# Performance work log

Measured on AMD Instinct MI355X. Metric: run time of the kernel, lower is better.

Reference implementation:

```python
import jax, jax.numpy as jnp
import numpy as np

B, L, D, H = 4, 2048, 1024, 16
HD = D // H


def setup_inputs() -> dict:
    key = jax.random.key(0)
    k0, k1, k2, k3, k4 = jax.random.split(key, 5)
    scale = 1.0 / np.sqrt(D)
    x = jax.random.normal(k0, (B, L, D), dtype=jnp.float32)
    Wk = jax.random.normal(k1, (D, D), dtype=jnp.float32) * scale
    Wv = jax.random.normal(k2, (D, D), dtype=jnp.float32) * scale
    Wr = jax.random.normal(k3, (D, D), dtype=jnp.float32) * scale
    Wo = jax.random.normal(k4, (D, D), dtype=jnp.float32) * scale
    # time_decay init: geometric decay per head, broadcast over head_dim
    decay = jnp.exp(-5.0 * jnp.arange(1, H + 1, dtype=jnp.float32) / H)
    time_decay = jnp.broadcast_to(decay[:, None], (H, HD)).astype(jnp.float32)
    time_first = jnp.full((H, HD), 0.5, dtype=jnp.float32)
    return {"x": x, "Wk": Wk, "Wv": Wv, "Wr": Wr, "Wo": Wo,
            "time_decay": time_decay, "time_first": time_first}


def reference(x, Wk, Wv, Wr, Wo, time_decay, time_first):
    b, l, d = x.shape
    h, hd = time_decay.shape
    # projections (nn.Linear: x @ W.T)
    k = (x @ Wk.T).reshape(b, l, h, hd)
    v = (x @ Wv.T).reshape(b, l, h, hd)
    r = jax.nn.sigmoid(x @ Wr.T).reshape(b, l, h, hd)

    decay = time_decay[None, :, :, None]   # (1,H,HD,1) broadcast over 'e' axis
    tf = time_first[None, :, :, None]      # (1,H,HD,1)

    def step(state, inp):
        k_t, v_t, r_t = inp                 # each (B,H,HD)
        # state: (B,H,HD,HD); outer product k_t (d) x v_t (e)
        state = state * decay + (k_t[..., :, None] * v_t[..., None, :]) * tf
        y_t = jnp.einsum('bhde,bhd->bhe', state, r_t)
        return state, y_t

    state0 = jnp.zeros((b, h, hd, hd), dtype=x.dtype)
    seq = (jnp.moveaxis(k, 1, 0), jnp.moveaxis(v, 1, 0), jnp.moveaxis(r, 1, 0))
    final_state, ys = jax.lax.scan(step, state0, seq)   # ys: (L,B,H,HD)
    y = jnp.moveaxis(ys, 0, 1).reshape(b, l, d) @ Wo.T
    return y, final_state
```

## Files before the change

kernel.cpp:

```cpp
#include <hip/hip_runtime.h>

typedef unsigned short u16;
typedef unsigned int   u32;
typedef __attribute__((ext_vector_type(8))) short bfrag;
typedef __attribute__((ext_vector_type(4))) float ffrag;

#define MFMA16(a,b,c) __builtin_amdgcn_mfma_f32_16x16x32_bf16((a),(b),(c),0,0,0)

#define GLL16(gp, lp) __builtin_amdgcn_global_load_lds( \
    (const __attribute__((address_space(1))) u32*)(gp), \
    (__attribute__((address_space(3))) u32*)(lp), 16, 0, 0)

__device__ __forceinline__ u16 f2b(float f) {
  u32 u = __float_as_uint(f);
  return (u16)((u + 0x7fffu + ((u >> 16) & 1u)) >> 16);
}
__device__ __forceinline__ float b2f(u16 v) { return __uint_as_float(((u32)v) << 16); }

__device__ __forceinline__ void unpack8(uint4 q, u16 e[8]) {
  e[0] = q.x & 0xffffu; e[1] = q.x >> 16;
  e[2] = q.y & 0xffffu; e[3] = q.y >> 16;
  e[4] = q.z & 0xffffu; e[5] = q.z >> 16;
  e[6] = q.w & 0xffffu; e[7] = q.w >> 16;
}

__global__ __launch_bounds__(256) void cvt_all(
    const float* __restrict__ x,  const float* __restrict__ wk,
    const float* __restrict__ wv, const float* __restrict__ wr,
    const float* __restrict__ wo,
    u16* __restrict__ xb, u16* __restrict__ wb, u16* __restrict__ wob)
{
  size_t i4 = ((size_t)blockIdx.x * 256 + threadIdx.x) * 4;
  const float* src; u16* dst; size_t off;
  if      (i4 <  8388608) { src = x;  dst = xb;            off = i4; }
  else if (i4 <  9437184) { src = wk; dst = wb;            off = i4 - 8388608; }
  else if (i4 < 10485760) { src = wv; dst = wb + 1048576;  off = i4 - 9437184; }
  else if (i4 < 11534336) { src = wr; dst = wb + 2097152;  off = i4 - 10485760; }
  else                    { src = wo; dst = wob;           off = i4 - 11534336; }
  float4 f = *(const float4*)(src + off);
  u16 o[4] = { f2b(f.x), f2b(f.y), f2b(f.z), f2b(f.w) };
  *(ushort4*)(dst + off) = make_ushort4(o[0], o[1], o[2], o[3]);
}

__global__ __launch_bounds__(512, 4) void k1_proj(
    const u16* __restrict__ xb, const u16* __restrict__ wb,
    const float* __restrict__ tf,
    u16* __restrict__ kws, u16* __restrict__ vws, u16* __restrict__ rws)
{
  __shared__ u16 As[2][256 * 32];
  __shared__ u16 Bs[2][128 * 32];
  const int tid  = threadIdx.x;
  const int wave = tid >> 6, lane = tid & 63;
  const int li = lane & 15, quad = lane >> 4;
  const int wm = (wave >> 1) * 64, wn = (wave & 1) * 64;

  const int bid = blockIdx.x;
  const int xcd = bid & 7, j = bid >> 3;
  const int n0 = (j >> 2) * 128;
  const int m0 = ((xcd << 2) | (j & 3)) * 256;

  ffrag acc[4][4];
#pragma unroll
  for (int i = 0; i < 4; ++i)
#pragma unroll
    for (int jj = 0; jj < 4; ++jj)
#pragma unroll
      for (int r = 0; r < 4; ++r) acc[i][jj][r] = 0.f;

  const int sr = lane >> 2, sc = (lane & 3) * 8;
  const u16* ga0 = xb + (size_t)(m0 + wave * 32 + sr) * 1024 + sc;
  const u16* gb0 = wb + (size_t)(n0 + wave * 16 + sr) * 1024 + sc;

  GLL16(ga0,             As[0] + wave * 1024);
  GLL16(ga0 + 16 * 1024, As[0] + wave * 1024 + 512);
  GLL16(gb0,             Bs[0] + wave * 512);

  for (int it = 0; it < 32; ++it) {
    __syncthreads();
    if (it + 1 < 32) {
      const int nb = (it + 1) & 1;
      const u16* ga = ga0 + (it + 1) * 32;
      const u16* gb = gb0 + (it + 1) * 32;
      GLL16(ga,             As[nb] + wave * 1024);
      GLL16(ga + 16 * 1024, As[nb] + wave * 1024 + 512);
      GLL16(gb,             Bs[nb] + wave * 512);
    }
    const int cb = it & 1;
    bfrag av[4], bv[4];
#pragma unroll
    for (int i = 0; i < 4; ++i)  av[i]  = *(const bfrag*)&As[cb][(wm + i * 16 + li) * 32 + quad * 8];
#pragma unroll
    for (int jj = 0; jj < 4; ++jj) bv[jj] = *(const bfrag*)&Bs[cb][(wn + jj * 16 + li) * 32 + quad * 8];
#pragma unroll
    for (int i = 0; i < 4; ++i)
#pragma unroll
      for (int jj = 0; jj < 4; ++jj)
        acc[i][jj] = MFMA16(av[i], bv[jj], acc[i][jj]);
  }

  const int sel = n0 >> 10;
#pragma unroll
  for (int i = 0; i < 4; ++i) {
#pragma unroll
    for (int jj = 0; jj < 4; ++jj) {
#pragma unroll
      for (int r = 0; r < 4; ++r) {
        int m = m0 + wm + i * 16 + quad * 4 + r;
        int n = n0 + wn + jj * 16 + li;
        int c = n & 1023;
        int bb = m >> 11, l = m & 2047;
        size_t dst = (size_t)((bb << 4) | (c >> 6)) * 131072 + (size_t)l * 64 + (c & 63);
        float v = acc[i][jj][r];
        if (sel == 0)      kws[dst] = f2b(v * tf[c]);
        else if (sel == 1) vws[dst] = f2b(v);
        else               rws[dst] = f2b(1.f / (1.f + __expf(-v)));
      }
    }
  }
}

#define ST 72

__global__ __launch_bounds__(256) void k2a_u(
    const u16* __restrict__ kws, const u16* __restrict__ vws,
    const float* __restrict__ td, u16* __restrict__ ut)
{
  __shared__ u16 KbarT[64 * ST];
  __shared__ u16 Vt[64 * ST];
  const int tid = threadIdx.x;
  const int lane = tid & 63, wave = tid >> 6;
  const int li = lane & 15, quad = lane >> 4;
  const int wr = (wave >> 1) * 32, wc = (wave & 1) * 32;
  const int bid = blockIdx.x;
  const int bh = bid >> 5, ch = bid & 31;
  const int h = bh & 15;
  const float l2D = log2f(td[h * 64]);
  const size_t base = (size_t)bh * 131072 + (size_t)ch * 4096;

#pragma unroll
  for (int it = 0; it < 2; ++it) {
    int c16 = tid + it * 256;
    int row = c16 >> 3, c8 = (c16 & 7) * 8;
    size_t g = base + (size_t)row * 64 + c8;
    uint4 kq = *(const uint4*)(kws + g);
    u16 ke[8]; unpack8(kq, ke);
    float sk = exp2f((float)(63 - row) * l2D);
#pragma unroll
    for (int jj = 0; jj < 8; ++jj) KbarT[(c8 + jj) * ST + row] = f2b(b2f(ke[jj]) * sk);
    uint4 vq = *(const uint4*)(vws + g);
    u16 ve[8]; unpack8(vq, ve);
#pragma unroll
    for (int jj = 0; jj < 8; ++jj) Vt[(c8 + jj) * ST + row] = ve[jj];
  }
  __syncthreads();

  ffrag U[2][2];
#pragma unroll
  for (int a = 0; a < 2; ++a)
#pragma unroll
    for (int b = 0; b < 2; ++b)
#pragma unroll
      for (int r = 0; r < 4; ++r) U[a][b][r] = 0.f;
#pragma unroll
  for (int kk = 0; kk < 64; kk += 32) {
    bfrag a0 = *(const bfrag*)&Vt[(wr + li) * ST + kk + quad * 8];
    bfrag a1 = *(const bfrag*)&Vt[(wr + 16 + li) * ST + kk + quad * 8];
    bfrag b0 = *(const bfrag*)&KbarT[(wc + li) * ST + kk + quad * 8];
    bfrag b1 = *(const bfrag*)&KbarT[(wc + 16 + li) * ST + kk + quad * 8];
    U[0][0] = MFMA16(a0, b0, U[0][0]);
    U[0][1] = MFMA16(a0, b1, U[0][1]);
    U[1][0] = MFMA16(a1, b0, U[1][0]);
    U[1][1] = MFMA16(a1, b1, U[1][1]);
  }

  u16* dst = ut + ((size_t)bid << 12);
#pragma unroll
  for (int ti = 0; ti < 2; ++ti)
#pragma unroll
    for (int tj = 0; tj < 2; ++tj)
#pragma unroll
      for (int r = 0; r < 4; ++r) {
        int e = wr + ti * 16 + quad * 4 + r;
        int d = wc + tj * 16 + li;
        dst[e * 64 + d] = f2b(U[ti][tj][r]);
      }
}

__global__ __launch_bounds__(256) void k2b_scan(
    const u16* __restrict__ ut, const float* __restrict__ td,
    u16* __restrict__ sbf, float* __restrict__ fstate)
{
  __shared__ float Sl[4 * 65];
  const int tid = threadIdx.x;
  const int bid = blockIdx.x;
  const int bh = bid >> 4, q = bid & 15;
  const int ed = q * 256 + tid;
  const int h = bh & 15;
  const float Dh = td[h * 64];
  const float DhC = exp2f(64.f * log2f(Dh));

  float S = 0.f;
  size_t idx = ((size_t)bh * 32) * 4096 + ed;
  for (int c = 0; c < 32; ++c, idx += 4096) {
    sbf[idx] = f2b(S);
    S = S * DhC + b2f(ut[idx]);
  }
  Sl[(tid >> 6) * 65 + (tid & 63)] = S;
  __syncthreads();
  int d = tid >> 2, el = tid & 3;
  fstate[(size_t)bh * 4096 + (size_t)d * 64 + q * 4 + el] = Sl[el * 65 + d];
}

__global__ __launch_bounds__(256) void k2c_y(
    const u16* __restrict__ kws, const u16* __restrict__ vws, const u16* __restrict__ rws,
    const u16* __restrict__ sbf, const float* __restrict__ td,
    u16* __restrict__ yws)
{
  __shared__ u16 Rc[64 * ST];
  __shared__ u16 KcA[64 * ST];
  __shared__ u16 Vt[64 * ST];
  __shared__ u16 STc[64 * ST];
  __shared__ float Dpow[65];

  const int tid = threadIdx.x;
  const int lane = tid & 63, wave = tid >> 6;
  const int li = lane & 15, quad = lane >> 4;
  const int wr = (wave >> 1) * 32, wc = (wave & 1) * 32;
  const int bid = blockIdx.x;
  const int bh = bid >> 5, ch = bid & 31;
  const int h = bh & 15, bb = bh >> 4;
  const float l2D = log2f(td[h * 64]);
  if (tid <= 64) Dpow[tid] = exp2f((float)tid * l2D);

  const size_t base = (size_t)bh * 131072 + (size_t)ch * 4096;
  const u16* sp = sbf + ((size_t)bid << 12);

#pragma unroll
  for (int it = 0; it < 2; ++it) {
    int c16 = tid + it * 256;
    int row = c16 >> 3, c8 = (c16 & 7) * 8;
    size_t g = base + (size_t)row * 64 + c8;
    *(uint4*)&Rc[row * ST + c8]  = *(const uint4*)(rws + g);
    *(uint4*)&KcA[row * ST + c8] = *(const uint4*)(kws + g);
    *(uint4*)&STc[row * ST + c8] = *(const uint4*)(sp + (size_t)row * 64 + c8);
    uint4 vq = *(const uint4*)(vws + g);
    u16 ve[8]; unpack8(vq, ve);
#pragma unroll
    for (int jj = 0; jj < 8; ++jj) Vt[(c8 + jj) * ST + row] = ve[jj];
  }
  __syncthreads();

  ffrag P[2][2], Y[2][2];
#pragma unroll
  for (int a = 0; a < 2; ++a)
#pragma unroll
    for (int b = 0; b < 2; ++b)
#pragma unroll
      for (int r = 0; r < 4; ++r) { P[a][b][r] = 0.f; Y[a][b][r] = 0.f; }

#pragma unroll
  for (int kk = 0; kk < 64; kk += 32) {
    bfrag a0 = *(const bfrag*)&Rc[(wr + li) * ST + kk + quad * 8];
    bfrag a1 = *(const bfrag*)&Rc[(wr + 16 + li) * ST + kk + quad * 8];
    bfrag b0 = *(const bfrag*)&KcA[(wc + li) * ST + kk + quad * 8];
    bfrag b1 = *(const bfrag*)&KcA[(wc + 16 + li) * ST + kk + quad * 8];
    P[0][0] = MFMA16(a0, b0, P[0][0]);
    P[0][1] = MFMA16(a0, b1, P[0][1]);
    P[1][0] = MFMA16(a1, b0, P[1][0]);
    P[1][1] = MFMA16(a1, b1, P[1][1]);
    bfrag s0 = *(const bfrag*)&STc[(wc + li) * ST + kk + quad * 8];
    bfrag s1 = *(const bfrag*)&STc[(wc + 16 + li) * ST + kk + quad * 8];
    Y[0][0] = MFMA16(a0, s0, Y[0][0]);
    Y[0][1] = MFMA16(a0, s1, Y[0][1]);
    Y[1][0] = MFMA16(a1, s0, Y[1][0]);
    Y[1][1] = MFMA16(a1, s1, Y[1][1]);
  }

#pragma unroll
  for (int ti = 0; ti < 2; ++ti)
#pragma unroll
    for (int tj = 0; tj < 2; ++tj)
#pragma unroll
      for (int r = 0; r < 4; ++r) {
        int t = wr + ti * 16 + quad * 4 + r;
        Y[ti][tj][r] *= Dpow[t + 1];
      }
  __syncthreads();

#pragma unroll
  for (int ti = 0; ti < 2; ++ti)
#pragma unroll
    for (int tj = 0; tj < 2; ++tj)
#pragma unroll
      for (int r = 0; r < 4; ++r) {
        int t = wr + ti * 16 + quad * 4 + r;
        int s = wc + tj * 16 + li;
        float v = (t >= s) ? P[ti][tj][r] * Dpow[t - s] : 0.f;
        KcA[t * ST + s] = f2b(v);
      }
  __syncthreads();

#pragma unroll
  for (int kk = 0; kk < 64; kk += 32) {
    bfrag aa0 = *(const bfrag*)&KcA[(wr + li) * ST + kk + quad * 8];
    bfrag aa1 = *(const bfrag*)&KcA[(wr + 16 + li) * ST + kk + quad * 8];
    bfrag vb0 = *(const bfrag*)&Vt[(wc + li) * ST + kk + quad * 8];
    bfrag vb1 = *(const bfrag*)&Vt[(wc + 16 + li) * ST + kk + quad * 8];
    Y[0][0] = MFMA16(aa0, vb0, Y[0][0]);
    Y[0][1] = MFMA16(aa0, vb1, Y[0][1]);
    Y[1][0] = MFMA16(aa1, vb0, Y[1][0]);
    Y[1][1] = MFMA16(aa1, vb1, Y[1][1]);
  }

#pragma unroll
  for (int ti = 0; ti < 2; ++ti)
#pragma unroll
    for (int tj = 0; tj < 2; ++tj)
#pragma unroll
      for (int r = 0; r < 4; ++r) {
        int t = wr + ti * 16 + quad * 4 + r;
        int e = wc + tj * 16 + li;
        yws[((size_t)(bb * 2048 + ch * 64 + t)) * 1024 + h * 64 + e] = f2b(Y[ti][tj][r]);
      }
}

__global__ __launch_bounds__(512, 4) void k3_out(
    const u16* __restrict__ yb, const u16* __restrict__ wob, float* __restrict__ out)
{
  __shared__ u16 As[2][256 * 32];
  __shared__ u16 Bs[2][128 * 32];
  const int tid  = threadIdx.x;
  const int wave = tid >> 6, lane = tid & 63;
  const int li = lane & 15, quad = lane >> 4;
  const int wm = (wave >> 1) * 64, wn = (wave & 1) * 64;

  const int bid = blockIdx.x;
  const int xcd = bid & 7, j = bid >> 3;
  const int n0 = (j >> 2) * 128;
  const int m0 = ((xcd << 2) | (j & 3)) * 256;

  ffrag acc[4][4];
#pragma unroll
  for (int i = 0; i < 4; ++i)
#pragma unroll
    for (int jj = 0; jj < 4; ++jj)
#pragma unroll
      for (int r = 0; r < 4; ++r) acc[i][jj][r] = 0.f;

  const int sr = lane >> 2, sc = (lane & 3) * 8;
  const u16* ga0 = yb  + (size_t)(m0 + wave * 32 + sr) * 1024 + sc;
  const u16* gb0 = wob + (size_t)(n0 + wave * 16 + sr) * 1024 + sc;

  GLL16(ga0,             As[0] + wave * 1024);
  GLL16(ga0 + 16 * 1024, As[0] + wave * 1024 + 512);
  GLL16(gb0,             Bs[0] + wave * 512);

  for (int it = 0; it < 32; ++it) {
    __syncthreads();
    if (it + 1 < 32) {
      const int nb = (it + 1) & 1;
      const u16* ga = ga0 + (it + 1) * 32;
      const u16* gb = gb0 + (it + 1) * 32;
      GLL16(ga,             As[nb] + wave * 1024);
      GLL16(ga + 16 * 1024, As[nb] + wave * 1024 + 512);
      GLL16(gb,             Bs[nb] + wave * 512);
    }
    const int cb = it & 1;
    bfrag av[4], bv[4];
#pragma unroll
    for (int i = 0; i < 4; ++i)  av[i]  = *(const bfrag*)&As[cb][(wm + i * 16 + li) * 32 + quad * 8];
#pragma unroll
    for (int jj = 0; jj < 4; ++jj) bv[jj] = *(const bfrag*)&Bs[cb][(wn + jj * 16 + li) * 32 + quad * 8];
#pragma unroll
    for (int i = 0; i < 4; ++i)
#pragma unroll
      for (int jj = 0; jj < 4; ++jj)
        acc[i][jj] = MFMA16(av[i], bv[jj], acc[i][jj]);
  }

#pragma unroll
  for (int i = 0; i < 4; ++i)
#pragma unroll
    for (int jj = 0; jj < 4; ++jj)
#pragma unroll
      for (int r = 0; r < 4; ++r) {
        int m = m0 + wm + i * 16 + quad * 4 + r;
        int n = n0 + wn + jj * 16 + li;
        out[(size_t)m * 1024 + n] = acc[i][jj][r];
      }
}

extern "C" void kernel_launch(void* const* d_in, const int* in_sizes, int n_in,
                              void* d_out, int out_size, void* d_ws, size_t ws_size,
                              hipStream_t stream) {
  const float* x  = (const float*)d_in[0];
  const float* Wk = (const float*)d_in[1];
  const float* Wv = (const float*)d_in[2];
  const float* Wr = (const float*)d_in[3];
  const float* Wo = (const float*)d_in[4];
  const float* td = (const float*)d_in[5];
  const float* tf = (const float*)d_in[6];
  float* out = (float*)d_out;

  u16* ws  = (u16*)d_ws;
  u16* xb  = ws;
  u16* wb  = ws + 8388608;
  u16* wob = ws + 11534336;
  u16* kws = ws + 12582912;
  u16* vws = ws + 20971520;
  u16* rws = ws + 29360128;
  u16* ut  = ws + 37748736;
  u16* sbf = ws + 54525952;
  u16* yws = xb;

  hipLaunchKernelGGL(cvt_all, dim3(12288), dim3(256), 0, stream,
                     x, Wk, Wv, Wr, Wo, xb, wb, wob);
  hipLaunchKernelGGL(k1_proj, dim3(768), dim3(512), 0, stream,
                     xb, wb, tf, kws, vws, rws);
  hipLaunchKernelGGL(k2a_u, dim3(2048), dim3(256), 0, stream,
                     kws, vws, td, ut);
  hipLaunchKernelGGL(k2b_scan, dim3(1024), dim3(256), 0, stream,
                     ut, td, sbf, out + 8388608);
  hipLaunchKernelGGL(k2c_y, dim3(2048), dim3(256), 0, stream,
                     kws, vws, rws, sbf, td, yws);
  hipLaunchKernelGGL(k3_out, dim3(256), dim3(512), 0, stream,
                     yws, wob, out);
}
```

Measured before the change: 237.0 us.

## Store GEMM LDS tiles in MFMA fragment order and pre-transpose V for k2c

Both GEMM kernels now map lanes to row = lane&15 and k-chunk = lane>>4 in their global_load_lds copies. Each 16x32 slab then lands in LDS already in MFMA fragment order, so each operand read is one contiguous lane-linear 16-byte load instead of a row-strided access that can conflict on banks. Separately, k2a_u writes its already-transposed V tile into a new workspace region. k2c_y then loads V with vector copies instead of unpacking and scattering 2-byte transposed stores into LDS. The cost is extra global write and read traffic for the V^T buffer.

```diff
diff --git a/kernel.cpp b/kernel.cpp
--- a/kernel.cpp
+++ b/kernel.cpp
@@ -67,13 +67,16 @@
 #pragma unroll
       for (int r = 0; r < 4; ++r) acc[i][jj][r] = 0.f;
 
-  const int sr = lane >> 2, sc = (lane & 3) * 8;
-  const u16* ga0 = xb + (size_t)(m0 + wave * 32 + sr) * 1024 + sc;
-  const u16* gb0 = wb + (size_t)(n0 + wave * 16 + sr) * 1024 + sc;
+  const int srow = lane & 15, scol = (lane >> 4) * 8;
+  const u16* ga0 = xb + (size_t)(m0 + wave * 32 + srow) * 1024 + scol;
+  const u16* gb0 = wb + (size_t)(n0 + wave * 16 + srow) * 1024 + scol;
 
   GLL16(ga0,             As[0] + wave * 1024);
   GLL16(ga0 + 16 * 1024, As[0] + wave * 1024 + 512);
   GLL16(gb0,             Bs[0] + wave * 512);
+
+  const int agrp = (wave >> 1) * 4;
+  const int bgrp = (wave & 1) * 4;
 
   for (int it = 0; it < 32; ++it) {
     __syncthreads();
@@ -88,9 +91,9 @@
     const int cb = it & 1;
     bfrag av[4], bv[4];
 #pragma unroll
-    for (int i = 0; i < 4; ++i)  av[i]  = *(const bfrag*)&As[cb][(wm + i * 16 + li) * 32 + quad * 8];
-#pragma unroll
-    for (int jj = 0; jj < 4; ++jj) bv[jj] = *(const bfrag*)&Bs[cb][(wn + jj * 16 + li) * 32 + quad * 8];
+    for (int i = 0; i < 4; ++i)  av[i]  = *(const bfrag*)&As[cb][(agrp + i) * 512 + lane * 8];
+#pragma unroll
+    for (int jj = 0; jj < 4; ++jj) bv[jj] = *(const bfrag*)&Bs[cb][(bgrp + jj) * 512 + lane * 8];
 #pragma unroll
     for (int i = 0; i < 4; ++i)
 #pragma unroll
@@ -123,7 +126,7 @@
 
 __global__ __launch_bounds__(256) void k2a_u(
     const u16* __restrict__ kws, const u16* __restrict__ vws,
-    const float* __restrict__ td, u16* __restrict__ ut)
+    const float* __restrict__ td, u16* __restrict__ ut, u16* __restrict__ vtw)
 {
   __shared__ u16 KbarT[64 * ST];
   __shared__ u16 Vt[64 * ST];
@@ -173,6 +176,14 @@
     U[1][1] = MFMA16(a1, b1, U[1][1]);
   }
 
+  u16* vdst = vtw + ((size_t)bid << 12);
+#pragma unroll
+  for (int it = 0; it < 2; ++it) {
+    int idx = tid + it * 256;
+    int e = idx >> 3, s8 = (idx & 7) * 8;
+    *(uint4*)(vdst + (size_t)e * 64 + s8) = *(const uint4*)&Vt[e * ST + s8];
+  }
+
   u16* dst = ut + ((size_t)bid << 12);
 #pragma unroll
   for (int ti = 0; ti < 2; ++ti)
@@ -212,7 +223,7 @@
 }
 
 __global__ __launch_bounds__(256) void k2c_y(
-    const u16* __restrict__ kws, const u16* __restrict__ vws, const u16* __restrict__ rws,
+    const u16* __restrict__ kws, const u16* __restrict__ vtw, const u16* __restrict__ rws,
     const u16* __restrict__ sbf, const float* __restrict__ td,
     u16* __restrict__ yws)
 {
@@ -234,19 +245,18 @@
 
   const size_t base = (size_t)bh * 131072 + (size_t)ch * 4096;
   const u16* sp = sbf + ((size_t)bid << 12);
+  const u16* vp = vtw + ((size_t)bid << 12);
 
 #pragma unroll
   for (int it = 0; it < 2; ++it) {
     int c16 = tid + it * 256;
     int row = c16 >> 3, c8 = (c16 & 7) * 8;
     size_t g = base + (size_t)row * 64 + c8;
+    size_t lo = (size_t)row * 64 + c8;
     *(uint4*)&Rc[row * ST + c8]  = *(const uint4*)(rws + g);
     *(uint4*)&KcA[row * ST + c8] = *(const uint4*)(kws + g);
-    *(uint4*)&STc[row * ST + c8] = *(const uint4*)(sp + (size_t)row * 64 + c8);
-    uint4 vq = *(const uint4*)(vws + g);
-    u16 ve[8]; unpack8(vq, ve);
-#pragma unroll
-    for (int jj = 0; jj < 8; ++jj) Vt[(c8 + jj) * ST + row] = ve[jj];
+    *(uint4*)&Vt[row * ST + c8]  = *(const uint4*)(vp + lo);
+    *(uint4*)&STc[row * ST + c8] = *(const uint4*)(sp + lo);
   }
   __syncthreads();
 
@@ -347,13 +357,16 @@
 #pragma unroll
       for (int r = 0; r < 4; ++r) acc[i][jj][r] = 0.f;
 
-  const int sr = lane >> 2, sc = (lane & 3) * 8;
-  const u16* ga0 = yb  + (size_t)(m0 + wave * 32 + sr) * 1024 + sc;
-  const u16* gb0 = wob + (size_t)(n0 + wave * 16 + sr) * 1024 + sc;
+  const int srow = lane & 15, scol = (lane >> 4) * 8;
+  const u16* ga0 = yb  + (size_t)(m0 + wave * 32 + srow) * 1024 + scol;
+  const u16* gb0 = wob + (size_t)(n0 + wave * 16 + srow) * 1024 + scol;
 
   GLL16(ga0,             As[0] + wave * 1024);
   GLL16(ga0 + 16 * 1024, As[0] + wave * 1024 + 512);
   GLL16(gb0,             Bs[0] + wave * 512);
+
+  const int agrp = (wave >> 1) * 4;
+  const int bgrp = (wave & 1) * 4;
 
   for (int it = 0; it < 32; ++it) {
     __syncthreads();
@@ -368,9 +381,9 @@
     const int cb = it & 1;
     bfrag av[4], bv[4];
 #pragma unroll
-    for (int i = 0; i < 4; ++i)  av[i]  = *(const bfrag*)&As[cb][(wm + i * 16 + li) * 32 + quad * 8];
-#pragma unroll
-    for (int jj = 0; jj < 4; ++jj) bv[jj] = *(const bfrag*)&Bs[cb][(wn + jj * 16 + li) * 32 + quad * 8];
+    for (int i = 0; i < 4; ++i)  av[i]  = *(const bfrag*)&As[cb][(agrp + i) * 512 + lane * 8];
+#pragma unroll
+    for (int jj = 0; jj < 4; ++jj) bv[jj] = *(const bfrag*)&Bs[cb][(bgrp + jj) * 512 + lane * 8];
 #pragma unroll
     for (int i = 0; i < 4; ++i)
 #pragma unroll
@@ -410,6 +423,7 @@
   u16* vws = ws + 20971520;
   u16* rws = ws + 29360128;
   u16* ut  = ws + 37748736;
+  u16* vtw = ws + 46137344;
   u16* sbf = ws + 54525952;
   u16* yws = xb;
 
@@ -418,11 +432,11 @@
   hipLaunchKernelGGL(k1_proj, dim3(768), dim3(512), 0, stream,
                      xb, wb, tf, kws, vws, rws);
   hipLaunchKernelGGL(k2a_u, dim3(2048), dim3(256), 0, stream,
-                     kws, vws, td, ut);
+                     kws, vws, td, ut, vtw);
   hipLaunchKernelGGL(k2b_scan, dim3(1024), dim3(256), 0, stream,
                      ut, td, sbf, out + 8388608);
   hipLaunchKernelGGL(k2c_y, dim3(2048), dim3(256), 0, stream,
-                     kws, vws, rws, sbf, td, yws);
+                     kws, vtw, rws, sbf, td, yws);
   hipLaunchKernelGGL(k3_out, dim3(256), dim3(512), 0, stream,
                      yws, wob, out);
 }
```

After: 261.6 us. 10.3% more time.
